# Kernel tuning notes

Measured on AMD Instinct MI355X. Metric: run time of the kernel, lower is better.

## Reference

```python
import jax, jax.numpy as jnp
import numpy as np

B, S, H = 2, 2048, 3072
NQ, NKV, HD = 24, 8, 128
ROT = 96  # floor(128 * 0.75)
BASE = 10000.0


def _rope(x, rotary_dim, base=BASE, start_index=0):
    # x: [b, s, h, rotary_dim]; keras_hub GPT-NeoX style half-rotation
    s = x.shape[1]
    inv_freq = 1.0 / (base ** (jnp.arange(0, rotary_dim, 2, dtype=jnp.float32) / rotary_dim))
    pos = jnp.arange(s, dtype=jnp.float32) + start_index
    freq = pos[:, None] * inv_freq[None, :]            # [s, rot/2]
    emb = jnp.concatenate([freq, freq], axis=-1)       # [s, rot]
    cos = jnp.cos(emb)[None, :, None, :]
    sin = jnp.sin(emb)[None, :, None, :]
    x1, x2 = jnp.split(x, 2, axis=-1)
    half_rot = jnp.concatenate([-x2, x1], axis=-1)
    return x * cos + half_rot * sin


def setup_inputs() -> dict:
    key = jax.random.key(0)
    k1, k2, k3, k4, k5 = jax.random.split(key, 5)
    hidden_states = jax.random.normal(k1, (B, S, H), dtype=jnp.float32)
    # causal mask [B, S, S]
    attention_mask = jnp.broadcast_to(jnp.tril(jnp.ones((S, S), dtype=bool)), (B, S, S))
    scale = 0.02
    Wq = jax.random.normal(k2, (H, NQ, HD), dtype=jnp.float32) * scale
    Wk = jax.random.normal(k3, (H, NKV, HD), dtype=jnp.float32) * scale
    Wv = jax.random.normal(k4, (H, NKV, HD), dtype=jnp.float32) * scale
    Wo = jax.random.normal(k5, (NQ, HD, H), dtype=jnp.float32) * scale
    return {"hidden_states": hidden_states, "attention_mask": attention_mask,
            "Wq": Wq, "Wk": Wk, "Wv": Wv, "Wo": Wo}


def reference(hidden_states, attention_mask, Wq, Wk, Wv, Wo):
    groups = NQ // NKV
    inv_norm = 1.0 / np.sqrt(HD)
    q = jnp.einsum('bqm,muh->bquh', hidden_states, Wq)   # [B,S,NQ,HD]
    k = jnp.einsum('bkm,mvh->bkvh', hidden_states, Wk)   # [B,S,NKV,HD]
    v = jnp.einsum('bkm,mvh->bkvh', hidden_states, Wv)
    # partial RoPE on first ROT dims
    q = jnp.concatenate([_rope(q[..., :ROT], ROT), q[..., ROT:]], axis=-1)
    k = jnp.concatenate([_rope(k[..., :ROT], ROT), k[..., ROT:]], axis=-1)
    # GQA: repeat kv heads (interleaved, matches ops.repeat axis=2)
    k = jnp.repeat(k, groups, axis=2)
    v = jnp.repeat(v, groups, axis=2)
    scores = jnp.einsum('bquh,bkuh->buqk', q, k) * inv_norm  # [B,NQ,S,S]
    scores = scores.astype(jnp.float32)
    scores = jnp.where(attention_mask[:, None, :, :], scores, -1e9)
    probs = jax.nn.softmax(scores, axis=-1).astype(hidden_states.dtype)
    attn = jnp.einsum('buqk,bkuh->bquh', probs, v)           # [B,S,NQ,HD]
    return jnp.einsum('bquh,uhm->bqm', attn, Wo)             # [B,S,H]
```

## Files before the change

kernel.cpp:

```cpp
#include <hip/hip_runtime.h>
#include <hip/hip_bf16.h>
#include <cstdint>

namespace {

constexpr int Bn = 2, Sn = 2048, Hn = 3072, NQn = 24, NKVn = 8, HDn = 128;
constexpr int LDQKV = NQn * HDn + 2 * NKVn * HDn;
constexpr int KCOLo = NQn * HDn;
constexpr int VCOLo = KCOLo + NKVn * HDn;

typedef __attribute__((ext_vector_type(8))) __bf16 bf16x8;
typedef __attribute__((ext_vector_type(4))) float f32x4;
typedef __attribute__((ext_vector_type(4))) unsigned short u16x4;

__device__ __forceinline__ unsigned short f2bf(float f) {
  union { float f; unsigned u; } v; v.f = f;
  return (unsigned short)((v.u + 0x7fffu + ((v.u >> 16) & 1u)) >> 16);
}
__device__ __forceinline__ float bf2f(unsigned short u) {
  union { unsigned u; float f; } v; v.u = ((unsigned)u) << 16;
  return v.f;
}
__device__ __forceinline__ void gload_lds16(const void* g, void* l) {
  __builtin_amdgcn_global_load_lds(
      (__attribute__((address_space(1))) void*)(uintptr_t)g,
      (__attribute__((address_space(3))) void*)(uintptr_t)l, 16, 0, 0);
}

__global__ void build_rope_tab(float* __restrict__ cosT, float* __restrict__ sinT) {
  int idx = blockIdx.x * 256 + threadIdx.x;
  if (idx >= Sn * 48) return;
  int s = idx / 48, i = idx % 48;
  float invf = exp2f(-(float)i * (13.287712379549449f / 48.f));
  float f = (float)s * invf;
  cosT[idx] = cosf(f);
  sinT[idx] = sinf(f);
}

__global__ void cvt_f32_bf16(const float* __restrict__ in, unsigned short* __restrict__ out, int n) {
  int i = (blockIdx.x * 256 + threadIdx.x) * 4;
  int stride = gridDim.x * 256 * 4;
  for (; i < n; i += stride) {
    float4 v = *(const float4*)&in[i];
    u16x4 o;
    o[0] = f2bf(v.x); o[1] = f2bf(v.y); o[2] = f2bf(v.z); o[3] = f2bf(v.w);
    *(u16x4*)&out[i] = o;
  }
}

__global__ void transpose_cvt(const float* __restrict__ in, unsigned short* __restrict__ out,
                              int K, int N) {
  __shared__ float tile[32][33];
  int bx = blockIdx.x * 32;
  int by = blockIdx.y * 32;
  int tx = threadIdx.x & 31, ty = threadIdx.x >> 5;
#pragma unroll
  for (int r = ty; r < 32; r += 8)
    tile[r][tx] = in[(size_t)(by + r) * N + bx + tx];
  __syncthreads();
#pragma unroll
  for (int r = ty; r < 32; r += 8)
    out[(size_t)(bx + r) * K + by + tx] = f2bf(tile[tx][r]);
}

__global__ void transpose_v(const unsigned short* __restrict__ QKV, unsigned short* __restrict__ VT) {
  __shared__ unsigned short tile[32][33];
  int s0 = blockIdx.x * 32;
  int b = blockIdx.y >> 5;
  int vc0 = (blockIdx.y & 31) * 32;
  int tx = threadIdx.x & 31, ty = threadIdx.x >> 5;
#pragma unroll
  for (int r = ty; r < 32; r += 8)
    tile[r][tx] = QKV[(size_t)(b * Sn + s0 + r) * LDQKV + VCOLo + vc0 + tx];
  __syncthreads();
#pragma unroll
  for (int r = ty; r < 32; r += 8)
    VT[(size_t)(b * (NKVn * HDn) + vc0 + r) * Sn + s0 + tx] = tile[tx][r];
}

template <int BF16OUT>
__launch_bounds__(256, 2)
__global__ void gemm_tn(const unsigned short* __restrict__ A, const unsigned short* __restrict__ Bm,
                        void* __restrict__ Cout, int M, int N, int K) {
  __shared__ unsigned short Atile[128 * 32];
  __shared__ unsigned short Btile[128 * 32];
  const int t = threadIdx.x;
  const int lane = t & 63, w = t >> 6;
  const int wr = w >> 1, wc = w & 1;
  const int brow = blockIdx.y * 128, bcol = blockIdx.x * 128;
  f32x4 acc[4][4] = {};
  const int nK = K >> 5;
  const int r0 = t >> 2, ko0 = (t & 3) * 8;
  const unsigned short* Ab = A + (size_t)brow * K;
  const unsigned short* Bb = Bm + (size_t)bcol * K;
  char* Al0 = (char*)Atile + w * 1024;
  char* Al1 = (char*)Atile + 4096 + w * 1024;
  char* Bl0 = (char*)Btile + w * 1024;
  char* Bl1 = (char*)Btile + 4096 + w * 1024;
  const int l15 = lane & 15, lk = (lane >> 4) * 8;

  for (int kt = 0; kt < nK; ++kt) {
    const int k0 = kt * 32;
    __syncthreads();
    gload_lds16(Ab + (size_t)r0 * K + k0 + ko0, Al0);
    gload_lds16(Ab + (size_t)(r0 + 64) * K + k0 + ko0, Al1);
    gload_lds16(Bb + (size_t)r0 * K + k0 + ko0, Bl0);
    gload_lds16(Bb + (size_t)(r0 + 64) * K + k0 + ko0, Bl1);
    __syncthreads();
    bf16x8 aF[4], bF[4];
#pragma unroll
    for (int m = 0; m < 4; ++m)
      aF[m] = *(const bf16x8*)&Atile[(wr * 64 + m * 16 + l15) * 32 + lk];
#pragma unroll
    for (int n = 0; n < 4; ++n)
      bF[n] = *(const bf16x8*)&Btile[(wc * 64 + n * 16 + l15) * 32 + lk];
#pragma unroll
    for (int m = 0; m < 4; ++m)
#pragma unroll
      for (int n = 0; n < 4; ++n)
        acc[m][n] = __builtin_amdgcn_mfma_f32_16x16x32_bf16(aF[m], bF[n], acc[m][n], 0, 0, 0);
  }
  const int lr = (lane >> 4) * 4, lc = lane & 15;
  if (BF16OUT) {
    unsigned short* C = (unsigned short*)Cout;
#pragma unroll
    for (int m = 0; m < 4; ++m) {
      int row = brow + wr * 64 + m * 16 + lr;
#pragma unroll
      for (int n = 0; n < 4; ++n) {
        int col = bcol + wc * 64 + n * 16 + lc;
#pragma unroll
        for (int i = 0; i < 4; ++i)
          C[(size_t)(row + i) * N + col] = f2bf(acc[m][n][i]);
      }
    }
  } else {
    float* C = (float*)Cout;
#pragma unroll
    for (int m = 0; m < 4; ++m) {
      int row = brow + wr * 64 + m * 16 + lr;
#pragma unroll
      for (int n = 0; n < 4; ++n) {
        int col = bcol + wc * 64 + n * 16 + lc;
#pragma unroll
        for (int i = 0; i < 4; ++i)
          C[(size_t)(row + i) * N + col] = acc[m][n][i];
      }
    }
  }
}

__global__ void rope_kernel(unsigned short* __restrict__ QKV, const float* __restrict__ cosT,
                            const float* __restrict__ sinT) {
  int rid = blockIdx.x;
  int s = rid & (Sn - 1);
  unsigned short* row = QKV + (size_t)rid * LDQKV;
  for (int p = threadIdx.x; p < 32 * 48; p += 256) {
    int h = p / 48, i = p % 48;
    int col = (h < NQn) ? h * HDn : KCOLo + (h - NQn) * HDn;
    float c = cosT[s * 48 + i], sn = sinT[s * 48 + i];
    float x1 = bf2f(row[col + i]), x2 = bf2f(row[col + i + 48]);
    row[col + i] = f2bf(x1 * c - x2 * sn);
    row[col + i + 48] = f2bf(x2 * c + x1 * sn);
  }
}

__launch_bounds__(256, 2)
__global__ void attn_kernel(const unsigned short* __restrict__ QKV,
                            const unsigned short* __restrict__ VT,
                            unsigned short* __restrict__ O) {
  __shared__ unsigned short Klds[2][64 * 128];
  __shared__ unsigned short Vlds[2][128 * 64];
  __shared__ unsigned short Plds[4][16 * 64];
  const int t = threadIdx.x, lane = t & 63, w = t >> 6;
  const int bq = gridDim.x - 1 - blockIdx.x;
  const int hid = blockIdx.y;
  const int b = hid / NQn, u = hid % NQn, kv = u / 3;
  const int l15 = lane & 15, lh = lane >> 4;

  bf16x8 qf[4];
  {
    int qrow = bq * 64 + w * 16 + l15;
    const unsigned short* qp = QKV + (size_t)(b * Sn + qrow) * LDQKV + u * HDn;
#pragma unroll
    for (int f = 0; f < 4; ++f) qf[f] = *(const bf16x8*)(qp + f * 32 + lh * 8);
  }
  float mrow[4], lrow[4];
  f32x4 Oa[8] = {};
#pragma unroll
  for (int i = 0; i < 4; ++i) { mrow[i] = -1e30f; lrow[i] = 0.f; }
  const float cscale = 0.08838834764831845f * 1.4426950408889634f;

  const unsigned short* Kg = QKV + (size_t)(b * Sn) * LDQKV + KCOLo + kv * HDn;
  const unsigned short* Vg = VT + (size_t)(b * NKVn + kv) * HDn * Sn;

  auto stageK = [&](int kt, int buf) {
#pragma unroll
    for (int iter = 0; iter < 4; ++iter) {
      int c = iter * 256 + t;
      int krow = c >> 4, pch = c & 15;
      int hch = (pch & 8) | ((pch & 7) ^ (krow & 7));
      gload_lds16(Kg + (size_t)(kt * 64 + krow) * LDQKV + hch * 8,
                  (char*)&Klds[buf][0] + (iter * 256 + w * 64) * 16);
    }
  };
  auto stageV = [&](int kt, int buf) {
#pragma unroll
    for (int iter = 0; iter < 4; ++iter) {
      int c = iter * 256 + t;
      int hd = c >> 3, p = c & 7;
      int sch = p ^ (hd & 7);
      gload_lds16(Vg + (size_t)hd * Sn + kt * 64 + sch * 8,
                  (char*)&Vlds[buf][0] + (iter * 256 + w * 64) * 16);
    }
  };

  const int nt = bq + 1;
  stageK(0, 0);
  stageV(0, 0);
  __syncthreads();

  for (int kt = 0; kt < nt; ++kt) {
    const int cur = kt & 1;
    if (kt + 1 < nt) { stageK(kt + 1, cur ^ 1); stageV(kt + 1, cur ^ 1); }
    const unsigned short* Kb = &Klds[cur][0];
    const unsigned short* Vb = &Vlds[cur][0];
    f32x4 Sg[4] = {};
    __builtin_amdgcn_s_setprio(1);
#pragma unroll
    for (int g = 0; g < 4; ++g) {
      int kcol = g * 16 + l15;
#pragma unroll
      for (int s = 0; s < 4; ++s) {
        int h = s * 4 + lh;
        int p = (h & 8) | ((h & 7) ^ (kcol & 7));
        bf16x8 kf = *(const bf16x8*)&Kb[kcol * 128 + p * 8];
        Sg[g] = __builtin_amdgcn_mfma_f32_16x16x32_bf16(qf[s], kf, Sg[g], 0, 0, 0);
      }
    }
    __builtin_amdgcn_s_setprio(0);
    float P[4][4];
    const bool last = (kt == bq);
#pragma unroll
    for (int g = 0; g < 4; ++g)
#pragma unroll
      for (int i = 0; i < 4; ++i) {
        float sv = Sg[g][i] * cscale;
        if (last) {
          int colw = g * 16 + l15;
          int roww = w * 16 + lh * 4 + i;
          if (colw > roww) sv = -1e30f;
        }
        P[g][i] = sv;
      }
    float rs[4];
#pragma unroll
    for (int i = 0; i < 4; ++i) {
      float pm = fmaxf(fmaxf(P[0][i], P[1][i]), fmaxf(P[2][i], P[3][i]));
#pragma unroll
      for (int msk = 1; msk < 16; msk <<= 1) pm = fmaxf(pm, __shfl_xor(pm, msk, 64));
      float mn = fmaxf(mrow[i], pm);
      rs[i] = exp2f(mrow[i] - mn);
      mrow[i] = mn;
      float ps = 0.f;
#pragma unroll
      for (int g = 0; g < 4; ++g) { float e = exp2f(P[g][i] - mn); P[g][i] = e; ps += e; }
#pragma unroll
      for (int msk = 1; msk < 16; msk <<= 1) ps += __shfl_xor(ps, msk, 64);
      lrow[i] = lrow[i] * rs[i] + ps;
    }
#pragma unroll
    for (int g = 0; g < 8; ++g)
#pragma unroll
      for (int i = 0; i < 4; ++i) Oa[g][i] *= rs[i];
    unsigned short* pl = Plds[w];
#pragma unroll
    for (int g = 0; g < 4; ++g) {
      int k = g * 16 + l15, ch = k >> 3;
#pragma unroll
      for (int i = 0; i < 4; ++i) {
        int q = lh * 4 + i;
        int pos = (ch ^ (q & 7)) & 7;
        pl[q * 64 + pos * 8 + (k & 7)] = f2bf(P[g][i]);
      }
    }
    __builtin_amdgcn_s_setprio(1);
#pragma unroll
    for (int kk = 0; kk < 2; ++kk) {
      int ch = kk * 4 + lh;
      int posp = (ch ^ (l15 & 7)) & 7;
      bf16x8 pf = *(const bf16x8*)&pl[l15 * 64 + posp * 8];
#pragma unroll
      for (int g = 0; g < 8; ++g) {
        int hd = g * 16 + l15;
        int vpos = (ch ^ (hd & 7)) & 7;
        bf16x8 vf = *(const bf16x8*)&Vb[hd * 64 + vpos * 8];
        Oa[g] = __builtin_amdgcn_mfma_f32_16x16x32_bf16(pf, vf, Oa[g], 0, 0, 0);
      }
    }
    __builtin_amdgcn_s_setprio(0);
    __syncthreads();
  }
#pragma unroll
  for (int i = 0; i < 4; ++i) {
    float inv = 1.0f / lrow[i];
    int qrow = bq * 64 + w * 16 + lh * 4 + i;
    unsigned short* op = O + (size_t)(b * Sn + qrow) * (NQn * HDn) + u * HDn;
#pragma unroll
    for (int g = 0; g < 8; ++g) op[g * 16 + l15] = f2bf(Oa[g][i] * inv);
  }
}

}

extern "C" void kernel_launch(void* const* d_in, const int* in_sizes, int n_in,
                              void* d_out, int out_size, void* d_ws, size_t ws_size,
                              hipStream_t stream) {
  const float* hidden = (const float*)d_in[0];
  const float* Wq = (const float*)d_in[2];
  const float* Wk = (const float*)d_in[3];
  const float* Wv = (const float*)d_in[4];
  const float* Wo = (const float*)d_in[5];
  float* out = (float*)d_out;

  char* ws = (char*)d_ws;
  constexpr size_t szXb = (size_t)Bn * Sn * Hn * 2;
  constexpr size_t szWqkv = (size_t)LDQKV * Hn * 2;
  constexpr size_t szWo = (size_t)Hn * Hn * 2;
  constexpr size_t szVT = (size_t)Bn * NKVn * HDn * Sn * 2;
  constexpr size_t szQKV = (size_t)Bn * Sn * LDQKV * 2;
  constexpr size_t szTab = (size_t)Sn * 48 * 4;
  static_assert(szWo + szVT <= szWqkv, "Wob+VT must fit in Wqkv region");
  constexpr size_t szTotal = szXb + szWqkv + szQKV + 2 * szTab;
  if (ws_size < szTotal) return;

  unsigned short* Xb = (unsigned short*)(ws);
  unsigned short* Obuf = Xb;
  unsigned short* Wqkv = (unsigned short*)(ws + szXb);
  unsigned short* Wob = Wqkv;
  unsigned short* VT = (unsigned short*)(ws + szXb + szWo);
  unsigned short* QKV = (unsigned short*)(ws + szXb + szWqkv);
  float* cosT = (float*)(ws + szXb + szWqkv + szQKV);
  float* sinT = (float*)(ws + szXb + szWqkv + szQKV + szTab);

  build_rope_tab<<<(Sn * 48 + 255) / 256, 256, 0, stream>>>(cosT, sinT);
  cvt_f32_bf16<<<3072, 256, 0, stream>>>(hidden, Xb, Bn * Sn * Hn);
  transpose_cvt<<<dim3(96, 96), 256, 0, stream>>>(Wq, Wqkv, Hn, NQn * HDn);
  transpose_cvt<<<dim3(32, 96), 256, 0, stream>>>(Wk, Wqkv + (size_t)KCOLo * Hn, Hn, NKVn * HDn);
  transpose_cvt<<<dim3(32, 96), 256, 0, stream>>>(Wv, Wqkv + (size_t)VCOLo * Hn, Hn, NKVn * HDn);
  gemm_tn<1><<<dim3(LDQKV / 128, (Bn * Sn) / 128), 256, 0, stream>>>(Xb, Wqkv, QKV,
                                                                    Bn * Sn, LDQKV, Hn);
  transpose_cvt<<<dim3(96, 96), 256, 0, stream>>>(Wo, Wob, Hn, Hn);
  transpose_v<<<dim3(Sn / 32, Bn * NKVn * HDn / 32), 256, 0, stream>>>(QKV, VT);
  rope_kernel<<<Bn * Sn, 256, 0, stream>>>(QKV, cosT, sinT);
  attn_kernel<<<dim3(Sn / 64, Bn * NQn), 256, 0, stream>>>(QKV, VT, Obuf);
  gemm_tn<0><<<dim3(Hn / 128, (Bn * Sn) / 128), 256, 0, stream>>>(Obuf, Wob, out,
                                                                  Bn * Sn, Hn, Hn);
}
```

Baseline: 733.0 us.

## Transpose flash-attention MFMA outputs so each lane owns one query row

Swaps the MFMA operand order for both QK^T and PV so the accumulators hold S^T and O^T. Each lane then owns a single query row, so the online-softmax max and sum need only two cross-lane shuffles instead of four per row, and one scalar m/l state replaces four. P is written to LDS as packed 4-element vectors rather than scalar stores. The output goes through an LDS scratch tile (reusing Klds) so global stores become 16-byte coalesced row writes. The risk is that the new causal-mask indexing and the transposed layout must be exactly right, and the epilogue depends on Klds no longer being in use after the final loop barrier.

```diff
diff --git a/kernel.cpp b/kernel.cpp
--- a/kernel.cpp
+++ b/kernel.cpp
@@ -185,10 +185,8 @@
 #pragma unroll
     for (int f = 0; f < 4; ++f) qf[f] = *(const bf16x8*)(qp + f * 32 + lh * 8);
   }
-  float mrow[4], lrow[4];
+  float m_l = -1e30f, l_l = 0.f;
   f32x4 Oa[8] = {};
-#pragma unroll
-  for (int i = 0; i < 4; ++i) { mrow[i] = -1e30f; lrow[i] = 0.f; }
   const float cscale = 0.08838834764831845f * 1.4426950408889634f;
 
   const unsigned short* Kg = QKV + (size_t)(b * Sn) * LDQKV + KCOLo + kv * HDn;
@@ -235,79 +233,90 @@
         int h = s * 4 + lh;
         int p = (h & 8) | ((h & 7) ^ (kcol & 7));
         bf16x8 kf = *(const bf16x8*)&Kb[kcol * 128 + p * 8];
-        Sg[g] = __builtin_amdgcn_mfma_f32_16x16x32_bf16(qf[s], kf, Sg[g], 0, 0, 0);
+        Sg[g] = __builtin_amdgcn_mfma_f32_16x16x32_bf16(kf, qf[s], Sg[g], 0, 0, 0);
       }
     }
     __builtin_amdgcn_s_setprio(0);
     float P[4][4];
     const bool last = (kt == bq);
+    const int qin = w * 16 + l15;
 #pragma unroll
     for (int g = 0; g < 4; ++g)
 #pragma unroll
       for (int i = 0; i < 4; ++i) {
         float sv = Sg[g][i] * cscale;
-        if (last) {
-          int colw = g * 16 + l15;
-          int roww = w * 16 + lh * 4 + i;
-          if (colw > roww) sv = -1e30f;
-        }
+        if (last && (g * 16 + lh * 4 + i) > qin) sv = -1e30f;
         P[g][i] = sv;
       }
-    float rs[4];
-#pragma unroll
-    for (int i = 0; i < 4; ++i) {
-      float pm = fmaxf(fmaxf(P[0][i], P[1][i]), fmaxf(P[2][i], P[3][i]));
-#pragma unroll
-      for (int msk = 1; msk < 16; msk <<= 1) pm = fmaxf(pm, __shfl_xor(pm, msk, 64));
-      float mn = fmaxf(mrow[i], pm);
-      rs[i] = exp2f(mrow[i] - mn);
-      mrow[i] = mn;
-      float ps = 0.f;
-#pragma unroll
-      for (int g = 0; g < 4; ++g) { float e = exp2f(P[g][i] - mn); P[g][i] = e; ps += e; }
-#pragma unroll
-      for (int msk = 1; msk < 16; msk <<= 1) ps += __shfl_xor(ps, msk, 64);
-      lrow[i] = lrow[i] * rs[i] + ps;
-    }
+    float pmax = -1e30f;
+#pragma unroll
+    for (int g = 0; g < 4; ++g)
+#pragma unroll
+      for (int i = 0; i < 4; ++i) pmax = fmaxf(pmax, P[g][i]);
+    pmax = fmaxf(pmax, __shfl_xor(pmax, 16, 64));
+    pmax = fmaxf(pmax, __shfl_xor(pmax, 32, 64));
+    float mn = fmaxf(m_l, pmax);
+    float rs = exp2f(m_l - mn);
+    m_l = mn;
+    float ps = 0.f;
+#pragma unroll
+    for (int g = 0; g < 4; ++g)
+#pragma unroll
+      for (int i = 0; i < 4; ++i) {
+        float e = exp2f(P[g][i] - mn);
+        P[g][i] = e;
+        ps += e;
+      }
+    ps += __shfl_xor(ps, 16, 64);
+    ps += __shfl_xor(ps, 32, 64);
+    l_l = l_l * rs + ps;
 #pragma unroll
     for (int g = 0; g < 8; ++g)
 #pragma unroll
-      for (int i = 0; i < 4; ++i) Oa[g][i] *= rs[i];
+      for (int i = 0; i < 4; ++i) Oa[g][i] *= rs;
     unsigned short* pl = Plds[w];
 #pragma unroll
     for (int g = 0; g < 4; ++g) {
-      int k = g * 16 + l15, ch = k >> 3;
-#pragma unroll
-      for (int i = 0; i < 4; ++i) {
-        int q = lh * 4 + i;
-        int pos = (ch ^ (q & 7)) & 7;
-        pl[q * 64 + pos * 8 + (k & 7)] = f2bf(P[g][i]);
-      }
+      int ch = g * 2 + (lh >> 1);
+      int pos = ch ^ (l15 & 7);
+      u16x4 pk;
+#pragma unroll
+      for (int i = 0; i < 4; ++i) pk[i] = f2bf(P[g][i]);
+      *(u16x4*)&pl[l15 * 64 + pos * 8 + (lh & 1) * 4] = pk;
     }
     __builtin_amdgcn_s_setprio(1);
 #pragma unroll
     for (int kk = 0; kk < 2; ++kk) {
       int ch = kk * 4 + lh;
-      int posp = (ch ^ (l15 & 7)) & 7;
-      bf16x8 pf = *(const bf16x8*)&pl[l15 * 64 + posp * 8];
+      bf16x8 pf = *(const bf16x8*)&pl[l15 * 64 + ((ch ^ (l15 & 7)) & 7) * 8];
 #pragma unroll
       for (int g = 0; g < 8; ++g) {
         int hd = g * 16 + l15;
         int vpos = (ch ^ (hd & 7)) & 7;
         bf16x8 vf = *(const bf16x8*)&Vb[hd * 64 + vpos * 8];
-        Oa[g] = __builtin_amdgcn_mfma_f32_16x16x32_bf16(pf, vf, Oa[g], 0, 0, 0);
+        Oa[g] = __builtin_amdgcn_mfma_f32_16x16x32_bf16(vf, pf, Oa[g], 0, 0, 0);
       }
     }
     __builtin_amdgcn_s_setprio(0);
     __syncthreads();
   }
-#pragma unroll
-  for (int i = 0; i < 4; ++i) {
-    float inv = 1.0f / lrow[i];
-    int qrow = bq * 64 + w * 16 + lh * 4 + i;
-    unsigned short* op = O + (size_t)(b * Sn + qrow) * (NQn * HDn) + u * HDn;
-#pragma unroll
-    for (int g = 0; g < 8; ++g) op[g * 16 + l15] = f2bf(Oa[g][i] * inv);
+  {
+    unsigned short* sc = (unsigned short*)Klds + w * 2176;
+    float inv = 1.0f / l_l;
+#pragma unroll
+    for (int g = 0; g < 8; ++g)
+#pragma unroll
+      for (int i = 0; i < 4; ++i)
+        sc[l15 * 136 + g * 16 + lh * 4 + i] = f2bf(Oa[g][i] * inv);
+    int q = lane >> 2, a = lane & 3;
+    int row = bq * 64 + w * 16 + q;
+    unsigned short* op = O + (size_t)(b * Sn + row) * (NQn * HDn) + u * HDn;
+    const unsigned short* scr = sc + q * 136;
+#pragma unroll
+    for (int j = 0; j < 4; ++j) {
+      bf16x8 v = *(const bf16x8*)&scr[a * 8 + j * 32];
+      *(bf16x8*)&op[a * 8 + j * 32] = v;
+    }
   }
 }
 
```

Result: faster. 667.6 us (-8.9%).
